# Kernel tuning notes

Hardware: AMD Instinct MI355X
Metric: run time of the kernel (lower is better)

Reference implementation:

```python
import jax, jax.numpy as jnp
import numpy as np

N_QUBITS = 12
DIM = 2 ** N_QUBITS  # 4096
N_LAYERS = 3
N_LABELS = 28
B = 1024
IN_DIM = 768

# PennyLane default.qubit convention: wire 0 is the most-significant bit.
_idx = np.arange(DIM)
_bits = (_idx[:, None] >> (N_QUBITS - 1 - np.arange(N_QUBITS))) & 1
_Z = (1.0 - 2.0 * _bits).astype(np.float32)  # (DIM, 12): eigenvalues of Z_q per basis state
_ZZ = np.stack([_Z[:, i] * _Z[:, i + 1] for i in range(N_QUBITS - 1)], axis=1)  # (DIM, 11)


def _apply_1q(state, U, q):
    # state: (B, DIM) complex; U: (2,2) shared or (B,2,2) per-sample
    b = state.shape[0]
    left, right = 2 ** q, 2 ** (N_QUBITS - q - 1)
    s = state.reshape(b, left, 2, right)
    if U.ndim == 2:
        s = jnp.einsum('ab,kxbj->kxaj', U, s)
    else:
        s = jnp.einsum('kab,kxbj->kxaj', U, s)
    return s.reshape(b, DIM)


def _apply_cnot(state, c, t):
    b = state.shape[0]
    s = state.reshape((b,) + (2,) * N_QUBITS)
    s = jnp.moveaxis(s, (c + 1, t + 1), (-2, -1))
    # flip target amplitudes where control bit == 1
    s = jnp.stack([s[..., 0, :], s[..., 1, ::-1]], axis=-2)
    s = jnp.moveaxis(s, (-2, -1), (c + 1, t + 1))
    return s.reshape(b, DIM)


def _ry_mats(angles):
    # angles: (B, 12) -> (B, 12, 2, 2) complex RY matrices
    c, s = jnp.cos(angles / 2), jnp.sin(angles / 2)
    U = jnp.stack([jnp.stack([c, -s], -1), jnp.stack([s, c], -1)], -2)
    return U.astype(jnp.complex64)


def _rot_mats(w):
    # w: (12, 3) -> (12, 2, 2); qml.Rot(phi, theta, omega) = RZ(omega) RY(theta) RZ(phi)
    phi, theta, omega = w[:, 0], w[:, 1], w[:, 2]
    c = jnp.cos(theta / 2).astype(jnp.complex64)
    s = jnp.sin(theta / 2).astype(jnp.complex64)
    a = jnp.exp(-0.5j * (phi + omega)) * c
    bb = -jnp.exp(0.5j * (phi - omega)) * s
    cc = jnp.exp(-0.5j * (phi - omega)) * s
    d = jnp.exp(0.5j * (phi + omega)) * c
    return jnp.stack([jnp.stack([a, bb], -1), jnp.stack([cc, d], -1)], -2)


def _forward(x, W1, b1, ln_g, ln_b, W2, b2, qws, scales, biases):
    # --- DimensionalityReduction MLP (eval mode: dropout = identity) ---
    h = x @ W1.T + b1                                   # (B, 24)
    mu = h.mean(-1, keepdims=True)
    var = ((h - mu) ** 2).mean(-1, keepdims=True)
    h = (h - mu) / jnp.sqrt(var + 1e-5) * ln_g + ln_b   # LayerNorm
    h = jax.nn.relu(h)
    angles = jnp.tanh(h @ W2.T + b2)                    # (B, 12) in [-1, 1]

    # --- batched 12-qubit state-vector simulation ---
    state = jnp.zeros((angles.shape[0], DIM), jnp.complex64).at[:, 0].set(1.0)
    Ury = _ry_mats(angles)                              # (B, 12, 2, 2)
    for l in range(N_LAYERS):
        for q in range(N_QUBITS):                       # AngleEmbedding (RY, per sample)
            state = _apply_1q(state, Ury[:, q], q)
        R = _rot_mats(qws[l][0])                        # StronglyEntanglingLayers: Rot per qubit
        for q in range(N_QUBITS):
            state = _apply_1q(state, R[q], q)
        for q in range(N_QUBITS):                       # CNOT ring, range 1
            state = _apply_cnot(state, q, (q + 1) % N_QUBITS)

    probs = state.real ** 2 + state.imag ** 2           # (B, DIM)
    eZ = probs @ jnp.asarray(_Z)                        # (B, 12)
    eZZ = probs @ jnp.asarray(_ZZ)                      # (B, 11)
    eX = []
    for q in range(N_LABELS - N_QUBITS - (N_QUBITS - 1)):  # 5 PauliX observables
        left, right = 2 ** q, 2 ** (N_QUBITS - q - 1)
        s = state.reshape(-1, left, 2, right)
        eX.append(2 * jnp.sum(s[:, :, 0, :].real * s[:, :, 1, :].real
                              + s[:, :, 0, :].imag * s[:, :, 1, :].imag, axis=(1, 2)))
    exps = jnp.concatenate([eZ, eZZ, jnp.stack(eX, -1)], axis=1)  # (B, 28)
    return exps * scales + biases


def setup_inputs() -> dict:
    key = jax.random.key(0)
    ks = jax.random.split(key, 8)
    x = jax.random.normal(ks[0], (B, IN_DIM), jnp.float32)
    W1 = jax.random.normal(ks[1], (2 * N_QUBITS, IN_DIM), jnp.float32) * 0.05
    b1 = jnp.zeros((2 * N_QUBITS,), jnp.float32)
    ln_g = jnp.ones((2 * N_QUBITS,), jnp.float32)
    ln_b = jnp.zeros((2 * N_QUBITS,), jnp.float32)
    W2 = jax.random.normal(ks[2], (N_QUBITS, 2 * N_QUBITS), jnp.float32) * 0.2
    b2 = jnp.zeros((N_QUBITS,), jnp.float32)
    qw0 = jax.random.normal(ks[3], (1, N_QUBITS, 3), jnp.float32) * 0.1
    qw1 = jax.random.normal(ks[4], (1, N_QUBITS, 3), jnp.float32) * 0.1
    qw2 = jax.random.normal(ks[5], (1, N_QUBITS, 3), jnp.float32) * 0.1
    scales = jnp.ones((N_LABELS,), jnp.float32)
    biases = jnp.zeros((N_LABELS,), jnp.float32)
    return {"x": x, "W1": W1, "b1": b1, "ln_g": ln_g, "ln_b": ln_b, "W2": W2,
            "b2": b2, "qw0": qw0, "qw1": qw1, "qw2": qw2,
            "scales": scales, "biases": biases}


def reference(x, W1, b1, ln_g, ln_b, W2, b2, qw0, qw1, qw2, scales, biases):
    return _forward(x, W1, b1, ln_g, ln_b, W2, b2, (qw0, qw1, qw2), scales, biases)
```

## Files before the change

kernel.cpp:

```cpp
#include <hip/hip_runtime.h>
#include <math.h>

#define NQ   12
#define BLK  512
#define IND  768
#define HD   24
#define NOBS 28
#define CSTR 22

typedef float    f32x2 __attribute__((ext_vector_type(2)));
typedef float    f32x4 __attribute__((ext_vector_type(4)));
typedef __fp16   f16x2 __attribute__((ext_vector_type(2)));
typedef _Float16 h8    __attribute__((ext_vector_type(8)));

__device__ __forceinline__ unsigned pkrtz(float x, float y) {
    f16x2 h = __builtin_amdgcn_cvt_pkrtz(x, y);
    unsigned u; __builtin_memcpy(&u, &h, 4); return u;
}
__device__ __forceinline__ f32x2 unpack2(unsigned u) {
    f16x2 h; __builtin_memcpy(&h, &u, 4);
    f32x2 v; v.x = (float)h.x; v.y = (float)h.y; return v;
}
__device__ __forceinline__ f32x2 pk_cmul(f32x2 m, f32x2 u) {
    f32x2 r;
    asm("v_pk_mul_f32 %0, %1, %2 op_sel:[0,0] op_sel_hi:[0,1]"
        : "=v"(r) : "v"(m), "v"(u));
    asm("v_pk_fma_f32 %0, %1, %2, %0 op_sel:[1,1,0] op_sel_hi:[1,0,1] neg_lo:[0,1,0]"
        : "+v"(r) : "v"(m), "v"(u));
    return r;
}
__device__ __forceinline__ void pk_fma_plain(f32x2& acc, f32x2 a, f32x2 b) {
    asm("v_pk_fma_f32 %0, %1, %2, %0" : "+v"(acc) : "v"(a), "v"(b));
}
__device__ __forceinline__ h8 as_h8(uint4 u) { h8 r; __builtin_memcpy(&r, &u, 16); return r; }

__device__ __forceinline__ int pfx12(int y) { y ^= y >> 1; y ^= y >> 2; y ^= y >> 4; y ^= y >> 8; return y; }
__device__ __forceinline__ int pfx8 (int y) { y ^= y >> 1; y ^= y >> 2; y ^= y >> 4; return y; }

template<int LI, int G, int WM>
__device__ __forceinline__ void gstage(unsigned* st, const float GM[3][NQ][8],
                                       int l, int w) {
    const int a  = l & 15;
    const int mb = (l >> 4) * 4;

    unsigned A0u[4], A1u[4];
    #pragma unroll
    for (int bi = 0; bi < 4; ++bi) {
        const int bq = mb + bi;
        f32x2 u;
        {
            const float* F = GM[LI][11 - 4*G];
            const int off = (a & 1) * 4 + (bq & 1) * 2;
            u.x = F[off]; u.y = F[off + 1];
        }
        #pragma unroll
        for (int p = 1; p < 4; ++p) {
            const float* F = GM[LI][11 - 4*G - p];
            const int off = ((a >> p) & 1) * 4 + ((bq >> p) & 1) * 2;
            f32x2 e; e.x = F[off]; e.y = F[off + 1];
            u = pk_cmul(e, u);
        }
        A0u[bi] = pkrtz(u.x, -u.y);
        A1u[bi] = pkrtz(u.y,  u.x);
    }
    uint4 A04; A04.x = A0u[0]; A04.y = A0u[1]; A04.z = A0u[2]; A04.w = A0u[3];
    uint4 A14; A14.x = A1u[0]; A14.y = A1u[1]; A14.z = A1u[2]; A14.w = A1u[3];
    const h8 A0 = as_h8(A04), A1 = as_h8(A14);

    __syncthreads();
    uint2 B0[2], B1[2];
    #pragma unroll
    for (int tt = 0; tt < 2; ++tt) {
        const int base = (16 * (2*w + tt) + a) * CSTR + mb;
        B0[tt] = *(const uint2*)(st + base);
        B1[tt] = *(const uint2*)(st + base + 2);
    }
    __syncthreads();

    int TL = 0;
    if (WM >= 2) TL = pfx12(mb << 8);
    const int CTJ[4] = {0, 0x1FF, 0x3FF, 0x200};

    #pragma unroll
    for (int tt = 0; tt < 2; ++tt) {
        uint4 b4; b4.x = B0[tt].x; b4.y = B0[tt].y; b4.z = B1[tt].x; b4.w = B1[tt].y;
        f32x4 c0 = {0.f, 0.f, 0.f, 0.f}, c1 = {0.f, 0.f, 0.f, 0.f};
        const h8 Bh = as_h8(b4);
        c0 = __builtin_amdgcn_mfma_f32_16x16x32_f16(A0, Bh, c0, 0, 0, 0);
        c1 = __builtin_amdgcn_mfma_f32_16x16x32_f16(A1, Bh, c1, 0, 0, 0);
        const int n  = 16 * (2*w + tt) + a;
        const int TN = (WM >= 2) ? (pfx8(n) ^ TL) : 0;
        #pragma unroll
        for (int j = 0; j < 4; ++j) {
            const int m = mb + j;
            int addr;
            if (WM == 0)      addr = (m | (n & 0xF0)) * CSTR + (n & 15);
            else if (WM == 1) addr = ((n & 15) | (m << 4)) * CSTR + (n >> 4);
            else {
                const int tz = TN ^ CTJ[j];
                const int jp = tz ^ ((tz & 1) << 11);
                addr = (WM == 2) ? ((jp >> 4) * CSTR + (jp & 15))
                                 : ((jp & 255) * CSTR + (jp >> 8));
            }
            st[addr] = pkrtz(c0[j], c1[j]);
        }
    }
}

__global__ void __launch_bounds__(BLK, 4) pqm_kernel(
    const float* __restrict__ x,   const float* __restrict__ W1,
    const float* __restrict__ b1,  const float* __restrict__ ln_g,
    const float* __restrict__ ln_b,const float* __restrict__ W2,
    const float* __restrict__ b2,  const float* __restrict__ qw0,
    const float* __restrict__ qw1, const float* __restrict__ qw2,
    const float* __restrict__ scales, const float* __restrict__ biases,
    float* __restrict__ out)
{
    __shared__ unsigned st[256 * CSTR];
    __shared__ float GM[3][NQ][8];
    __shared__ float hb[HD];
    __shared__ float ang[2 * NQ];
    __shared__ float wpar[8][22];

    const int t   = threadIdx.x;
    const int w   = t >> 6;
    const int l   = t & 63;
    const int row = blockIdx.x;

    float* xs = (float*)st;
    if (t < 192) ((float4*)xs)[t] = ((const float4*)(x + row * IND))[t];
    __syncthreads();

    {
        int g = t >> 4, l16 = t & 15;
        if (g < HD) {
            const float* wp = W1 + g * IND;
            float acc = 0.f;
            #pragma unroll
            for (int k = 0; k < 12; ++k) {
                const int f4 = l16 + 16 * k;
                float4 a4 = ((const float4*)xs)[f4];
                float4 w4 = *(const float4*)(wp + 4 * f4);
                acc += a4.x * w4.x + a4.y * w4.y + a4.z * w4.z + a4.w * w4.w;
            }
            acc += __shfl_down(acc, 8, 16);
            acc += __shfl_down(acc, 4, 16);
            acc += __shfl_down(acc, 2, 16);
            acc += __shfl_down(acc, 1, 16);
            if (l16 == 0) hb[g] = acc + b1[g];
        } else if (t >= 448 && t < 484) {
            int u = t - 448; int li = u / NQ, q = u % NQ;
            const float* qw = (li == 0) ? qw0 : ((li == 1) ? qw1 : qw2);
            float phi = qw[q*3+0], th = qw[q*3+1], om = qw[q*3+2];
            float c = cosf(0.5f*th), s = sinf(0.5f*th);
            float sp, cp, sm, cm;
            sincosf(0.5f*(phi+om), &sp, &cp);
            sincosf(0.5f*(phi-om), &sm, &cm);
            float* R = GM[li][q];
            R[0] =  cp*c;  R[1] = -sp*c;
            R[2] = -cm*s;  R[3] = -sm*s;
            R[4] =  cm*s;  R[5] = -sm*s;
            R[6] =  cp*c;  R[7] =  sp*c;
        }
    }
    __syncthreads();

    if (t < NQ) {
        float mu = 0.f;
        #pragma unroll
        for (int j = 0; j < HD; ++j) mu += hb[j];
        mu *= (1.f / HD);
        float var = 0.f;
        #pragma unroll
        for (int j = 0; j < HD; ++j) { float d = hb[j] - mu; var += d * d; }
        var *= (1.f / HD);
        float rinv = 1.f / sqrtf(var + 1e-5f);
        float acc = b2[t];
        #pragma unroll
        for (int j = 0; j < HD; ++j) {
            float hn = (hb[j] - mu) * rinv * ln_g[j] + ln_b[j];
            acc += fmaxf(hn, 0.f) * W2[t * HD + j];
        }
        float a = tanhf(acc);
        ang[t]      = cosf(0.5f * a);
        ang[NQ + t] = sinf(0.5f * a);
    }
    __syncthreads();
    if (t < 36) {
        int li = t / NQ, q = t % NQ;
        float* R = GM[li][q];
        float r0=R[0],r1=R[1],r2=R[2],r3=R[3],r4=R[4],r5=R[5],r6=R[6],r7=R[7];
        float cr = ang[q], sr = ang[NQ + q];
        R[0] =  r0*cr + r2*sr;  R[1] =  r1*cr + r3*sr;
        R[2] = -r0*sr + r2*cr;  R[3] = -r1*sr + r3*cr;
        R[4] =  r4*cr + r6*sr;  R[5] =  r5*cr + r7*sr;
        R[6] = -r4*sr + r6*cr;  R[7] = -r5*sr + r7*cr;
    }
    __syncthreads();

    {
        f32x2 v0[8];
        f32x2 lf; lf.x = 1.f; lf.y = 0.f;
        #pragma unroll
        for (int u = 0; u < 9; ++u) {
            const float* F = GM[0][8 - u];
            const int bit = (t >> u) & 1;
            f32x2 e; e.x = F[bit * 4]; e.y = F[bit * 4 + 1];
            lf = pk_cmul(e, lf);
        }
        {
            const float* F = GM[0][11];
            f32x2 e0; e0.x = F[0]; e0.y = F[1];
            f32x2 e1; e1.x = F[4]; e1.y = F[5];
            v0[0] = pk_cmul(e0, lf); v0[1] = pk_cmul(e1, lf);
        }
        #pragma unroll
        for (int b = 1; b < 3; ++b) {
            const float* F = GM[0][11 - b];
            f32x2 e0; e0.x = F[0]; e0.y = F[1];
            f32x2 e1; e1.x = F[4]; e1.y = F[5];
            #pragma unroll
            for (int r = 0; r < (1 << b); ++r) {
                v0[r | (1 << b)] = pk_cmul(e1, v0[r]);
                v0[r]            = pk_cmul(e0, v0[r]);
            }
        }
        const int TL = pfx12(t << 3);
        #pragma unroll
        for (int r = 0; r < 8; ++r) {
            const int tr = r ^ (r >> 1) ^ (r >> 2);
            const int tz = TL ^ tr;
            const int jp = tz ^ ((tz & 1) << 11);
            st[(jp >> 4) * CSTR + (jp & 15)] = pkrtz(v0[r].x, v0[r].y);
        }
    }

    gstage<1, 0, 0>(st, GM, l, w);
    gstage<1, 1, 1>(st, GM, l, w);
    gstage<1, 2, 2>(st, GM, l, w);
    gstage<2, 0, 0>(st, GM, l, w);
    gstage<2, 1, 1>(st, GM, l, w);
    gstage<2, 2, 3>(st, GM, l, w);
    __syncthreads();

    {
        const int R = t & 255, h = t >> 8;
        const int rowb = R * CSTR + 8 * h;
        f32x2 v[8];
        #pragma unroll
        for (int p = 0; p < 4; ++p) {
            uint2 raw = *(const uint2*)(st + rowb + 2 * p);
            v[2*p]   = unpack2(raw.x);
            v[2*p+1] = unpack2(raw.y);
        }
        float ex[5];
        #pragma unroll
        for (int q = 1; q <= 3; ++q) {
            f32x2 acc; acc.x = 0.f; acc.y = 0.f;
            const int m = 8 >> q;
            #pragma unroll
            for (int r = 0; r < 8; ++r) pk_fma_plain(acc, v[r], v[r ^ m]);
            ex[q] = acc.x + acc.y;
        }
        {
            f32x2 acc; acc.x = 0.f; acc.y = 0.f;
            const int pb = R * CSTR + 8 * (h ^ 1);
            #pragma unroll
            for (int p = 0; p < 4; ++p) {
                uint2 raw = *(const uint2*)(st + pb + 2 * p);
                pk_fma_plain(acc, v[2*p],   unpack2(raw.x));
                pk_fma_plain(acc, v[2*p+1], unpack2(raw.y));
            }
            ex[0] = acc.x + acc.y;
        }
        {
            f32x2 acc; acc.x = 0.f; acc.y = 0.f;
            const int pb = (R ^ 128) * CSTR + 8 * h;
            #pragma unroll
            for (int p = 0; p < 4; ++p) {
                uint2 raw = *(const uint2*)(st + pb + 2 * p);
                pk_fma_plain(acc, v[2*p],   unpack2(raw.x));
                pk_fma_plain(acc, v[2*p+1], unpack2(raw.y));
            }
            ex[4] = acc.x + acc.y;
        }

        #pragma unroll
        for (int r = 0; r < 8; ++r) v[r].x = v[r].x * v[r].x + v[r].y * v[r].y;
        #pragma unroll
        for (int lev = 0; lev < 3; ++lev) {
            const int m = 1 << lev;
            #pragma unroll
            for (int r = 0; r < 8; ++r)
                if (!(r & m)) { float A = v[r].x, B = v[r | m].x; v[r].x = A + B; v[r | m].x = A - B; }
        }

        float ch = v[0].x;
        #pragma unroll
        for (int lev = 0; lev < 6; ++lev) {
            float o = __shfl_xor(ch, 1 << lev, 64);
            ch = (l & (1 << lev)) ? (o - ch) : (ch + o);
        }
        auto wsum = [&](float s) {
            #pragma unroll
            for (int d = 1; d < 64; d <<= 1) s += __shfl_xor(s, d, 64);
            return s;
        };
        float W4 = wsum(v[4].x), W2 = wsum(v[2].x), W1s = wsum(v[1].x);
        float W6 = wsum(v[6].x), W3 = wsum(v[3].x);
        float e0 = wsum(ex[0]), e1 = wsum(ex[1]), e2 = wsum(ex[2]);
        float e3 = wsum(ex[3]), e4 = wsum(ex[4]);

        if      (l == 0) {
            wpar[w][0]  = ch;
            wpar[w][12] = W4;  wpar[w][13] = W2; wpar[w][14] = W1s;
            wpar[w][15] = W6;  wpar[w][16] = W3;
            wpar[w][17] = e0;  wpar[w][18] = e1; wpar[w][19] = e2;
            wpar[w][20] = e3;  wpar[w][21] = e4;
        }
        else if (l == 32) wpar[w][1]  = ch;
        else if (l == 16) wpar[w][2]  = ch;
        else if (l == 8)  wpar[w][3]  = ch;
        else if (l == 4)  wpar[w][4]  = ch;
        else if (l == 2)  wpar[w][5]  = ch;
        else if (l == 1)  wpar[w][6]  = ch;
        else if (l == 48) wpar[w][7]  = ch;
        else if (l == 24) wpar[w][8]  = ch;
        else if (l == 12) wpar[w][9]  = ch;
        else if (l == 6)  wpar[w][10] = ch;
        else if (l == 3)  wpar[w][11] = ch;
    }
    __syncthreads();

    if (t < NOBS) {
        const int oslot[NOBS] = {0,12,13,14, 0,0, 1,2,3,4,5,6,
                                 12,15,16,14, 0,1, 7,8,9,10,11,
                                 17,18,19,20,21};
        const int omw[NOBS]   = {4,0,0,0, 2,1, 0,0,0,0,0,0,
                                 4,0,0,2, 3,1, 0,0,0,0,0,
                                 0,0,0,0,0};
        const int sl = oslot[t], mw = omw[t];
        float s = 0.f;
        #pragma unroll
        for (int g = 0; g < 8; ++g) {
            float p = wpar[g][sl];
            s += (__popc(g & mw) & 1) ? -p : p;
        }
        out[row * NOBS + t] = s * scales[t] + biases[t];
    }
}

extern "C" void kernel_launch(void* const* d_in, const int* in_sizes, int n_in,
                              void* d_out, int out_size, void* d_ws, size_t ws_size,
                              hipStream_t stream) {
    const int Bn = in_sizes[0] / IND;
    pqm_kernel<<<dim3(Bn), dim3(BLK), 0, stream>>>(
        (const float*)d_in[0], (const float*)d_in[1], (const float*)d_in[2],
        (const float*)d_in[3], (const float*)d_in[4], (const float*)d_in[5],
        (const float*)d_in[6], (const float*)d_in[7], (const float*)d_in[8],
        (const float*)d_in[9], (const float*)d_in[10], (const float*)d_in[11],
        (float*)d_out);
}
```

Before: 27.90 us.

## Precompute MFMA A-fragments for all six gate stages into shared memory

Each gate stage used to rebuild its 16x16 Kronecker-product A fragment in every wave with a chain of complex multiplies. Now 384 threads build the fragments for all six stages once, in parallel, into a new LDS buffer, and each stage loads them with two 128-bit reads. The row stride shrinks from 22 to 20 so B fragments load as one aligned uint4, and the store addressing is simplified to base-plus-stride. This costs about 12 KB of extra LDS per block, which may lower occupancy, and the stride change may alter bank-conflict patterns.

```diff
diff --git a/kernel.cpp b/kernel.cpp
--- a/kernel.cpp
+++ b/kernel.cpp
@@ -6,7 +6,7 @@
 #define IND  768
 #define HD   24
 #define NOBS 28
-#define CSTR 22
+#define CSTR 20
 
 typedef float    f32x2 __attribute__((ext_vector_type(2)));
 typedef float    f32x4 __attribute__((ext_vector_type(4)));
@@ -37,72 +37,54 @@
 __device__ __forceinline__ int pfx12(int y) { y ^= y >> 1; y ^= y >> 2; y ^= y >> 4; y ^= y >> 8; return y; }
 __device__ __forceinline__ int pfx8 (int y) { y ^= y >> 1; y ^= y >> 2; y ^= y >> 4; return y; }
 
-template<int LI, int G, int WM>
-__device__ __forceinline__ void gstage(unsigned* st, const float GM[3][NQ][8],
+template<int S, int WM>
+__device__ __forceinline__ void gstage(unsigned* st, const unsigned* Afr,
                                        int l, int w) {
     const int a  = l & 15;
     const int mb = (l >> 4) * 4;
 
-    unsigned A0u[4], A1u[4];
+    __syncthreads();
+    const unsigned* Ap = Afr + (S * 64 + l) * 8;
+    const uint4 A04 = *(const uint4*)(Ap);
+    const uint4 A14 = *(const uint4*)(Ap + 4);
+    uint4 Bf[2];
     #pragma unroll
-    for (int bi = 0; bi < 4; ++bi) {
-        const int bq = mb + bi;
-        f32x2 u;
-        {
-            const float* F = GM[LI][11 - 4*G];
-            const int off = (a & 1) * 4 + (bq & 1) * 2;
-            u.x = F[off]; u.y = F[off + 1];
-        }
-        #pragma unroll
-        for (int p = 1; p < 4; ++p) {
-            const float* F = GM[LI][11 - 4*G - p];
-            const int off = ((a >> p) & 1) * 4 + ((bq >> p) & 1) * 2;
-            f32x2 e; e.x = F[off]; e.y = F[off + 1];
-            u = pk_cmul(e, u);
-        }
-        A0u[bi] = pkrtz(u.x, -u.y);
-        A1u[bi] = pkrtz(u.y,  u.x);
-    }
-    uint4 A04; A04.x = A0u[0]; A04.y = A0u[1]; A04.z = A0u[2]; A04.w = A0u[3];
-    uint4 A14; A14.x = A1u[0]; A14.y = A1u[1]; A14.z = A1u[2]; A14.w = A1u[3];
+    for (int tt = 0; tt < 2; ++tt)
+        Bf[tt] = *(const uint4*)(st + (16 * (2*w + tt) + a) * CSTR + mb);
+    __syncthreads();
+
     const h8 A0 = as_h8(A04), A1 = as_h8(A14);
-
-    __syncthreads();
-    uint2 B0[2], B1[2];
-    #pragma unroll
-    for (int tt = 0; tt < 2; ++tt) {
-        const int base = (16 * (2*w + tt) + a) * CSTR + mb;
-        B0[tt] = *(const uint2*)(st + base);
-        B1[tt] = *(const uint2*)(st + base + 2);
-    }
-    __syncthreads();
-
     int TL = 0;
     if (WM >= 2) TL = pfx12(mb << 8);
     const int CTJ[4] = {0, 0x1FF, 0x3FF, 0x200};
 
     #pragma unroll
     for (int tt = 0; tt < 2; ++tt) {
-        uint4 b4; b4.x = B0[tt].x; b4.y = B0[tt].y; b4.z = B1[tt].x; b4.w = B1[tt].y;
         f32x4 c0 = {0.f, 0.f, 0.f, 0.f}, c1 = {0.f, 0.f, 0.f, 0.f};
-        const h8 Bh = as_h8(b4);
+        const h8 Bh = as_h8(Bf[tt]);
         c0 = __builtin_amdgcn_mfma_f32_16x16x32_f16(A0, Bh, c0, 0, 0, 0);
         c1 = __builtin_amdgcn_mfma_f32_16x16x32_f16(A1, Bh, c1, 0, 0, 0);
-        const int n  = 16 * (2*w + tt) + a;
-        const int TN = (WM >= 2) ? (pfx8(n) ^ TL) : 0;
-        #pragma unroll
-        for (int j = 0; j < 4; ++j) {
-            const int m = mb + j;
-            int addr;
-            if (WM == 0)      addr = (m | (n & 0xF0)) * CSTR + (n & 15);
-            else if (WM == 1) addr = ((n & 15) | (m << 4)) * CSTR + (n >> 4);
-            else {
+        const int n = 16 * (2*w + tt) + a;
+        if (WM == 0) {
+            const int base = (mb + (n & 0xF0)) * CSTR + (n & 15);
+            #pragma unroll
+            for (int j = 0; j < 4; ++j)
+                st[base + j * CSTR] = pkrtz(c0[j], c1[j]);
+        } else if (WM == 1) {
+            const int base = ((n & 15) + mb * 16) * CSTR + (n >> 4);
+            #pragma unroll
+            for (int j = 0; j < 4; ++j)
+                st[base + j * 16 * CSTR] = pkrtz(c0[j], c1[j]);
+        } else {
+            const int TN = pfx8(n) ^ TL;
+            #pragma unroll
+            for (int j = 0; j < 4; ++j) {
                 const int tz = TN ^ CTJ[j];
                 const int jp = tz ^ ((tz & 1) << 11);
-                addr = (WM == 2) ? ((jp >> 4) * CSTR + (jp & 15))
-                                 : ((jp & 255) * CSTR + (jp >> 8));
-            }
-            st[addr] = pkrtz(c0[j], c1[j]);
+                const int addr = (WM == 2) ? ((jp >> 4) * CSTR + (jp & 15))
+                                           : ((jp & 255) * CSTR + (jp >> 8));
+                st[addr] = pkrtz(c0[j], c1[j]);
+            }
         }
     }
 }
@@ -117,6 +99,7 @@
     float* __restrict__ out)
 {
     __shared__ unsigned st[256 * CSTR];
+    __shared__ unsigned Afr[6 * 64 * 8];
     __shared__ float GM[3][NQ][8];
     __shared__ float hb[HD];
     __shared__ float ang[2 * NQ];
@@ -198,6 +181,32 @@
     }
     __syncthreads();
 
+    if (t < 384) {
+        const int s = t >> 6, lane = t & 63;
+        const int LI = 1 + s / 3, G = s % 3;
+        const int a = lane & 15, mb = (lane >> 4) * 4;
+        unsigned* Ap = Afr + (s * 64 + lane) * 8;
+        #pragma unroll
+        for (int bi = 0; bi < 4; ++bi) {
+            const int bq = mb + bi;
+            f32x2 u;
+            {
+                const float* F = GM[LI][11 - 4*G];
+                const int off = (a & 1) * 4 + (bq & 1) * 2;
+                u.x = F[off]; u.y = F[off + 1];
+            }
+            #pragma unroll
+            for (int p = 1; p < 4; ++p) {
+                const float* F = GM[LI][11 - 4*G - p];
+                const int off = ((a >> p) & 1) * 4 + ((bq >> p) & 1) * 2;
+                f32x2 e; e.x = F[off]; e.y = F[off + 1];
+                u = pk_cmul(e, u);
+            }
+            Ap[bi]     = pkrtz(u.x, -u.y);
+            Ap[4 + bi] = pkrtz(u.y,  u.x);
+        }
+    }
+
     {
         f32x2 v0[8];
         f32x2 lf; lf.x = 1.f; lf.y = 0.f;
@@ -235,12 +244,12 @@
         }
     }
 
-    gstage<1, 0, 0>(st, GM, l, w);
-    gstage<1, 1, 1>(st, GM, l, w);
-    gstage<1, 2, 2>(st, GM, l, w);
-    gstage<2, 0, 0>(st, GM, l, w);
-    gstage<2, 1, 1>(st, GM, l, w);
-    gstage<2, 2, 3>(st, GM, l, w);
+    gstage<0, 0>(st, Afr, l, w);
+    gstage<1, 1>(st, Afr, l, w);
+    gstage<2, 2>(st, Afr, l, w);
+    gstage<3, 0>(st, Afr, l, w);
+    gstage<4, 1>(st, Afr, l, w);
+    gstage<5, 3>(st, Afr, l, w);
     __syncthreads();
 
     {
```

After: 26.63 us (median of 3 runs). 4.6% less time.
